# Kernel optimization log

Hardware: AMD Instinct MI355X
Metric: run time of the kernel (lower is better)

The kernel has to match this reference:

```python
import jax, jax.numpy as jnp
import numpy as np

TOK_DIM = 512
POS_DIM = 512
N_HEADS = 16
HEAD_DIM = 64
D_MODEL = 1024
INNER = N_HEADS * HEAD_DIM
B, T = 4, 2048


def setup_inputs() -> dict:
    key = jax.random.key(0)
    ks = jax.random.split(key, 5)
    s = 0.02
    return {
        "x": jax.random.normal(ks[0], (B, T, TOK_DIM + POS_DIM), dtype=jnp.float32),
        "Wq": jax.random.normal(ks[1], (POS_DIM, INNER), dtype=jnp.float32) * s,
        "Wk": jax.random.normal(ks[2], (POS_DIM, INNER), dtype=jnp.float32) * s,
        "Wv": jax.random.normal(ks[3], (TOK_DIM, INNER), dtype=jnp.float32) * s,
        "Wo": jax.random.normal(ks[4], (INNER, D_MODEL), dtype=jnp.float32) * s,
    }


def reference(x, Wq, Wk, Wv, Wo):
    b, t, _ = x.shape
    x_tok = x[:, :, :TOK_DIM]
    x_pos = x[:, :, TOK_DIM:]
    # project and split heads: [B, H, T, Dh]
    q = (x_pos @ Wq).reshape(b, t, N_HEADS, HEAD_DIM).transpose(0, 2, 1, 3)
    k = (x_pos @ Wk).reshape(b, t, N_HEADS, HEAD_DIM).transpose(0, 2, 1, 3)
    v = (x_tok @ Wv).reshape(b, t, N_HEADS, HEAD_DIM).transpose(0, 2, 1, 3)
    att = jnp.einsum("bhqd,bhkd->bhqk", q, k) / jnp.sqrt(jnp.float32(HEAD_DIM))
    causal = jnp.tril(jnp.ones((t, t), dtype=bool))
    att = jnp.where(causal, att, -jnp.inf)
    att = jax.nn.softmax(att, axis=-1)
    out = jnp.einsum("bhqk,bhkd->bhqd", att, v)
    out = out.transpose(0, 2, 1, 3).reshape(b, t, INNER)
    return out @ Wo
```

## Files before the change

### kernel.cpp

```cpp
#include <hip/hip_runtime.h>
#include <stdint.h>


typedef unsigned short u16;
typedef __bf16 bf16;
typedef bf16 bf16x8 __attribute__((ext_vector_type(8)));
typedef u16 u16x8 __attribute__((ext_vector_type(8)));
typedef u16 u16x4 __attribute__((ext_vector_type(4)));
typedef float f32x4 __attribute__((ext_vector_type(4)));
typedef uint32_t u32x4 __attribute__((ext_vector_type(4)));

__device__ __forceinline__ u16 cvt_bf16(float f) {
  uint32_t u = __builtin_bit_cast(uint32_t, f);
  u += 0x7FFFu + ((u >> 16) & 1u);
  return (u16)(u >> 16);
}

__device__ __forceinline__ f32x4 mfma_bf(bf16x8 a, bf16x8 b, f32x4 c) {
  return __builtin_amdgcn_mfma_f32_16x16x32_bf16(a, b, c, 0, 0, 0);
}

typedef __attribute__((address_space(1))) const uint32_t g_u32;
typedef __attribute__((address_space(3))) uint32_t l_u32;
__device__ __forceinline__ void gload16(const u16* g, u16* l) {
  __builtin_amdgcn_global_load_lds((g_u32*)g, (l_u32*)l, 16, 0, 0);
}

__global__ __launch_bounds__(256) void prep(
    const float* __restrict__ x, const float* __restrict__ Wq,
    const float* __restrict__ Wk, const float* __restrict__ Wv,
    const float* __restrict__ Wo, u16* __restrict__ xtok,
    u16* __restrict__ xpos, u16* __restrict__ Wt, u16* __restrict__ WoT) {
  const int gid = blockIdx.x;
  const int tid = threadIdx.x;
  if (gid < 1024) {
    const int z = gid >> 8;
    const float* src = (z == 0) ? Wq : (z == 1) ? Wk : (z == 2) ? Wv : Wo;
    const int K = (z == 3) ? 1024 : 512;
    u16* dst = (z == 3) ? WoT : (Wt + (size_t)z * 1024 * 512);
    const int k0 = ((gid >> 4) & 15) * 64, n0 = (gid & 15) * 64;
    if (k0 >= K) return;
    __shared__ u16 T[64][68];
    const int r = tid >> 4, c = (tid & 15) * 4;
#pragma unroll
    for (int i = 0; i < 4; i++) {
      float4 v = *(const float4*)(src + (size_t)(k0 + r + i * 16) * 1024 + n0 + c);
      u16x4 b = {cvt_bf16(v.x), cvt_bf16(v.y), cvt_bf16(v.z), cvt_bf16(v.w)};
      *(u16x4*)&T[r + i * 16][c] = b;
    }
    __syncthreads();
#pragma unroll
    for (int i = 0; i < 4; i++) {
      int n = r + i * 16;
      u16x4 v;
#pragma unroll
      for (int j = 0; j < 4; j++) v[j] = T[c + j][n];
      *(u16x4*)(dst + (size_t)(n0 + n) * K + k0 + c) = v;
    }
  } else {
    int idx = (gid - 1024) * 256 + tid;
    int row = idx >> 8;
    int c4 = (idx & 255) * 4;
    float4 v = *(const float4*)(x + (size_t)row * 1024 + c4);
    u16x4 b = {cvt_bf16(v.x), cvt_bf16(v.y), cvt_bf16(v.z), cvt_bf16(v.w)};
    u16* dst = (c4 < 512) ? (xtok + (size_t)row * 512 + c4)
                          : (xpos + (size_t)row * 512 + c4 - 512);
    *(u16x4*)dst = b;
  }
}


#define MM1(M_, N_, J_) { f32x4 c_ = acc[M_][N_];                            \
  c_ = mfma_bf(af[J_][0], bf[N_][0], c_);                                    \
  c_ = mfma_bf(af[J_][1], bf[N_][1], c_);                                    \
  acc[M_][N_] = c_; }

#define XMM(NB) MM1(0,(NB)+0,0) MM1(0,(NB)+1,0) MM1(1,(NB)+0,1)              \
                MM1(1,(NB)+1,1) MM1(2,(NB)+0,2) MM1(2,(NB)+1,2)              \
                MM1(3,(NB)+0,3) MM1(3,(NB)+1,3)

#define XLDA(P) { const u16* bp_ = rA + (P)*8192;                            \
  af[0][0] = *(const bf16x8*)(bp_ + 0*1024 + colx0);                         \
  af[0][1] = *(const bf16x8*)(bp_ + 0*1024 + colx1);                         \
  af[1][0] = *(const bf16x8*)(bp_ + 1*1024 + colx0);                         \
  af[1][1] = *(const bf16x8*)(bp_ + 1*1024 + colx1);                         \
  af[2][0] = *(const bf16x8*)(bp_ + 2*1024 + colx0);                         \
  af[2][1] = *(const bf16x8*)(bp_ + 2*1024 + colx1);                         \
  af[3][0] = *(const bf16x8*)(bp_ + 3*1024 + colx0);                         \
  af[3][1] = *(const bf16x8*)(bp_ + 3*1024 + colx1); }

#define XLDB(P, NB) { const u16* bp_ = rB + (P)*16384;                       \
  bf[(NB)+0][0] = *(const bf16x8*)(bp_ + ((NB)+0)*1024 + colx0);             \
  bf[(NB)+0][1] = *(const bf16x8*)(bp_ + ((NB)+0)*1024 + colx1);             \
  bf[(NB)+1][0] = *(const bf16x8*)(bp_ + ((NB)+1)*1024 + colx0);             \
  bf[(NB)+1][1] = *(const bf16x8*)(bp_ + ((NB)+1)*1024 + colx1); }

#define XSTA(P, KT) { const u16* s_ = gA + (KT)*64;                          \
  u16* d_ = lA + (P)*8192;                                                   \
  gload16(s_, d_); gload16(s_ + (size_t)64*Kd, d_ + 4096); }

#define XSTB0(P, KT) { const u16* s_ = gB + (KT)*64;                         \
  u16* d_ = lB + (P)*16384;                                                  \
  gload16(s_, d_); gload16(s_ + (size_t)64*Kd, d_ + 4096); }

#define XSTB1(P, KT) { const u16* s_ = gB + (size_t)128*Kd + (KT)*64;        \
  u16* d_ = lB + (P)*16384 + 8192;                                           \
  gload16(s_, d_); gload16(s_ + (size_t)64*Kd, d_ + 4096); }

#define PH_MID  asm volatile("" ::: "memory"); __builtin_amdgcn_s_barrier(); \
  asm volatile("s_waitcnt lgkmcnt(0)" ::: "memory");                         \
  __builtin_amdgcn_s_setprio(1);

#define PH_END_VM6  __builtin_amdgcn_s_setprio(0);                           \
  asm volatile("s_waitcnt vmcnt(6)" ::: "memory");                           \
  asm volatile("" ::: "memory"); __builtin_amdgcn_s_barrier();

template <int Kd>
__device__ __forceinline__ void gemm128_core(
    const u16* __restrict__ Aptr, const u16* __restrict__ Bptr,
    int m0, int n0, u16* smem, f32x4 (&acc)[4][4]) {
  constexpr int NKT = Kd / 64;
  const int tid = threadIdx.x;
  const int lane = tid & 63;
  const int mrow = lane & 15, quad = lane >> 4;
  const int w = tid >> 6, wm2 = w >> 2, wn4 = w & 3;

  u16* As = smem;
  u16* Bs = smem + 24576;

  const int lrs = tid >> 3, sp8 = tid & 7;
  const int slog = sp8 ^ (lrs & 7);
  const u16* gA = Aptr + (size_t)(m0 + lrs) * Kd + slog * 8;
  const u16* gB = Bptr + (size_t)(n0 + lrs) * Kd + slog * 8;
  u16* lA = As + tid * 8;
  u16* lB = Bs + tid * 8;

  const int colx0 = (quad * 8) ^ ((mrow & 7) * 8);
  const int colx1 = (32 + quad * 8) ^ ((mrow & 7) * 8);
  const u16* rA = As + (wm2 * 64 + mrow) * 64;
  const u16* rB = Bs + (wn4 >> 1) * 8192 + ((wn4 & 1) * 64 + mrow) * 64;

  bf16x8 af[4][2], bf[4][2];

  XSTA(0, 0) XSTB0(0, 0) XSTB1(0, 0)
  XSTA(1, 1) XSTB0(1, 1) XSTB1(1, 1)
  asm volatile("s_waitcnt vmcnt(6)" ::: "memory");
  asm volatile("" ::: "memory");
  __builtin_amdgcn_s_barrier();

  int p = 0, ps = 2;
  for (int t = 0; t < NKT; ++t) {
    const int kt = (t + 2 < NKT) ? t + 2 : NKT - 1;
    XLDA(p) XLDB(p, 0) XLDB(p, 2)
    XSTA(ps, kt) XSTB0(ps, kt) XSTB1(ps, kt)
    PH_MID
    XMM(0) XMM(2)
    PH_END_VM6
    p = (p == 2) ? 0 : p + 1;
    ps = (ps == 2) ? 0 : ps + 1;
  }
  asm volatile("s_waitcnt vmcnt(0)" ::: "memory");
  __builtin_amdgcn_s_barrier();
}

__device__ __forceinline__ void xcd_remap(int& bx, int& by) {
  int flat = blockIdx.x + 4 * blockIdx.y;
  int wg = (flat & 7) * 32 + (flat >> 3);
  bx = wg & 3;
  by = wg >> 2;
}

__global__ __launch_bounds__(512, 1) void gemm_qkv128(
    const u16* __restrict__ xtok, const u16* __restrict__ xpos,
    const u16* __restrict__ Wt, u16* __restrict__ qkv,
    u16* __restrict__ vperm) {
  const int z = blockIdx.z;
  const u16* A = (z == 2) ? xtok : xpos;
  const u16* Bt = Wt + (size_t)z * 1024 * 512;
  u16* outp = qkv + (size_t)z * (64u * 2048u * 64u);
  const float osc = (z == 0) ? 0.18033688011112042f : 1.0f;
  int bx, by;
  xcd_remap(bx, by);
  const int m0 = by * 128, n0 = bx * 256;

  __shared__ __align__(16) u16 smem[73728];
  f32x4 acc[4][4];
#pragma unroll
  for (int i = 0; i < 4; i++)
#pragma unroll
    for (int j = 0; j < 4; j++) acc[i][j] = (f32x4){0.f, 0.f, 0.f, 0.f};

  gemm128_core<512>(A, Bt, m0, n0, smem, acc);

  const int tid = threadIdx.x;
  const int lane = tid & 63;
  const int mrow = lane & 15, quad = lane >> 4;
  const int w = tid >> 6, wm2 = w >> 2, wn4 = w & 3;

  if (z != 2) {
#pragma unroll
    for (int mi = 0; mi < 4; mi++)
#pragma unroll
      for (int ni = 0; ni < 4; ni++)
#pragma unroll
        for (int r = 0; r < 4; r++) {
          int m = m0 + wm2 * 64 + mi * 16 + quad * 4 + r;
          int n = n0 + wn4 * 64 + ni * 16 + mrow;
          int bb = m >> 11, t = m & 2047;
          int h = n >> 6, d = n & 63;
          outp[(((size_t)(bb * 16 + h)) * 2048 + t) * 64 + d] =
              cvt_bf16(acc[mi][ni][r] * osc);
        }
  } else {
#pragma unroll
    for (int mi = 0; mi < 4; mi++)
#pragma unroll
      for (int ni = 0; ni < 4; ni++)
#pragma unroll
        for (int r = 0; r < 4; r++) {
          int m = m0 + wm2 * 64 + mi * 16 + quad * 4 + r;
          int n = n0 + wn4 * 64 + ni * 16 + mrow;
          int bb = m >> 11, t = m & 2047;
          int h = n >> 6, d = n & 63;
          int k6 = t & 63;
          int pos = (k6 & 32) + ((k6 >> 4) & 1) * 4 + ((k6 >> 2) & 3) * 8 +
                    (k6 & 3);
          vperm[(((size_t)(bb * 16 + h)) * 64 + d) * 2048 + (t & ~63) + pos] =
              cvt_bf16(acc[mi][ni][r]);
        }
  }
}

__global__ __launch_bounds__(512, 1) void gemm_out128(
    const u16* __restrict__ Am, const u16* __restrict__ WoT,
    float* __restrict__ out) {
  int bx, by;
  xcd_remap(bx, by);
  const int m0 = by * 128, n0 = bx * 256;

  __shared__ __align__(16) u16 smem[73728];
  f32x4 acc[4][4];
#pragma unroll
  for (int i = 0; i < 4; i++)
#pragma unroll
    for (int j = 0; j < 4; j++) acc[i][j] = (f32x4){0.f, 0.f, 0.f, 0.f};

  gemm128_core<1024>(Am, WoT, m0, n0, smem, acc);

  const int tid = threadIdx.x;
  const int lane = tid & 63;
  const int mrow = lane & 15, quad = lane >> 4;
  const int w = tid >> 6, wm2 = w >> 2, wn4 = w & 3;

#pragma unroll
  for (int mi = 0; mi < 4; mi++)
#pragma unroll
    for (int ni = 0; ni < 4; ni++)
#pragma unroll
      for (int r = 0; r < 4; r++) {
        int m = m0 + wm2 * 64 + mi * 16 + quad * 4 + r;
        int n = n0 + wn4 * 64 + ni * 16 + mrow;
        out[(size_t)m * 1024 + n] = acc[mi][ni][r];
      }
}

__global__ __launch_bounds__(256, 3) void attn(
    const u16* __restrict__ qkv, const u16* __restrict__ vperm,
    u16* __restrict__ aout) {
  const int bh = blockIdx.x;
  const int qt = 15 - blockIdx.y;
  const int bb = bh >> 4, h = bh & 15;
  const u16* Qp = qkv + (size_t)bh * (2048 * 64);
  const u16* Kp = qkv + (size_t)(64 + bh) * (2048 * 64);
  const u16* Vp = vperm + (size_t)bh * (64 * 2048);

  __shared__ __align__(16) u16 smem[2][4][64 * 32];

  const int tid = threadIdx.x;
  const int lane = tid & 63;
  const int w = tid >> 6;
  const int mrow = lane & 15;
  const int quad = lane >> 4;
  const int srow = w * 16 + (lane >> 2);
  const int sc = (lane & 3) * 8;
  const int soff = srow * 32 + sc;

  const u16x8 onesu = {0x3F80, 0x3F80, 0x3F80, 0x3F80,
                       0x3F80, 0x3F80, 0x3F80, 0x3F80};
  const bf16x8 ones = __builtin_bit_cast(bf16x8, onesu);

  const u16* kgb = Kp + (size_t)srow * 64 + sc;
  const u16* vgb = Vp + (size_t)srow * 2048 + sc;

  const int q0 = qt * 128;
  const int nk = 2 * qt + 2;
  const int qw = q0 + w * 32;

  const u16* qbase = Qp + (size_t)(qw + mrow) * 64 + quad * 8;
  const bf16x8 qf00 = *(const bf16x8*)qbase;
  const bf16x8 qf01 = *(const bf16x8*)(qbase + 32);
  const bf16x8 qf10 = *(const bf16x8*)(qbase + 16 * 64);
  const bf16x8 qf11 = *(const bf16x8*)(qbase + 16 * 64 + 32);

  f32x4 o[2][4], ol[2];
#pragma unroll
  for (int g = 0; g < 2; ++g) {
#pragma unroll
    for (int dt = 0; dt < 4; ++dt) o[g][dt] = (f32x4){0.f, 0.f, 0.f, 0.f};
    ol[g] = (f32x4){0.f, 0.f, 0.f, 0.f};
  }

  u16x8 ka0 = *(const u16x8*)kgb;
  u16x8 ka1 = *(const u16x8*)(kgb + 32);
  u16x8 va0 = *(const u16x8*)vgb;
  u16x8 va1 = *(const u16x8*)(vgb + 32);

  for (int it = 0; it < nk; ++it) {
    u16* buf = &smem[it & 1][0][0];
    *(u16x8*)(buf + 0 * 2048 + soff) = ka0;
    *(u16x8*)(buf + 1 * 2048 + soff) = ka1;
    *(u16x8*)(buf + 2 * 2048 + soff) = va0;
    *(u16x8*)(buf + 3 * 2048 + soff) = va1;

    if (it + 1 < nk) {
      const int kn = (it + 1) * 64;
      ka0 = *(const u16x8*)(kgb + (size_t)kn * 64);
      ka1 = *(const u16x8*)(kgb + (size_t)kn * 64 + 32);
      va0 = *(const u16x8*)(vgb + kn);
      va1 = *(const u16x8*)(vgb + kn + 32);
    }

    __syncthreads();

    const int k0 = it * 64;
    if (k0 > qw + 31) continue;

    f32x4 s[2][4];
#pragma unroll
    for (int nt = 0; nt < 4; ++nt) {
      bf16x8 kf0 = *(const bf16x8*)(buf + 0 * 2048 + (nt * 16 + mrow) * 32 + quad * 8);
      bf16x8 kf1 = *(const bf16x8*)(buf + 1 * 2048 + (nt * 16 + mrow) * 32 + quad * 8);
      f32x4 z0 = (f32x4){0.f, 0.f, 0.f, 0.f};
      z0 = mfma_bf(kf0, qf00, z0);
      s[0][nt] = mfma_bf(kf1, qf01, z0);
      f32x4 z1 = (f32x4){0.f, 0.f, 0.f, 0.f};
      z1 = mfma_bf(kf0, qf10, z1);
      s[1][nt] = mfma_bf(kf1, qf11, z1);
    }

    if (k0 + 63 > qw) {
#pragma unroll
      for (int g = 0; g < 2; ++g)
#pragma unroll
        for (int nt = 0; nt < 4; ++nt)
#pragma unroll
          for (int r = 0; r < 4; ++r)
            if (k0 + nt * 16 + quad * 4 + r > qw + g * 16 + mrow)
              s[g][nt][r] = -1e30f;
    }
#pragma unroll
    for (int g = 0; g < 2; ++g)
#pragma unroll
      for (int nt = 0; nt < 4; ++nt)
#pragma unroll
        for (int r = 0; r < 4; ++r)
          s[g][nt][r] = __builtin_amdgcn_exp2f(s[g][nt][r]);

    bf16x8 pf[2][2];
#pragma unroll
    for (int g = 0; g < 2; ++g) {
      pf[g][0] = (bf16x8){(bf16)s[g][0][0], (bf16)s[g][0][1],
                          (bf16)s[g][0][2], (bf16)s[g][0][3],
                          (bf16)s[g][1][0], (bf16)s[g][1][1],
                          (bf16)s[g][1][2], (bf16)s[g][1][3]};
      pf[g][1] = (bf16x8){(bf16)s[g][2][0], (bf16)s[g][2][1],
                          (bf16)s[g][2][2], (bf16)s[g][2][3],
                          (bf16)s[g][3][0], (bf16)s[g][3][1],
                          (bf16)s[g][3][2], (bf16)s[g][3][3]};
      ol[g] = mfma_bf(ones, pf[g][0], ol[g]);
      ol[g] = mfma_bf(ones, pf[g][1], ol[g]);
    }

#pragma unroll
    for (int dt = 0; dt < 4; ++dt) {
      bf16x8 vf0 = *(const bf16x8*)(buf + 2 * 2048 + (dt * 16 + mrow) * 32 + quad * 8);
      bf16x8 vf1 = *(const bf16x8*)(buf + 3 * 2048 + (dt * 16 + mrow) * 32 + quad * 8);
      o[0][dt] = mfma_bf(vf0, pf[0][0], o[0][dt]);
      o[0][dt] = mfma_bf(vf1, pf[0][1], o[0][dt]);
      o[1][dt] = mfma_bf(vf0, pf[1][0], o[1][dt]);
      o[1][dt] = mfma_bf(vf1, pf[1][1], o[1][dt]);
    }
  }

  __syncthreads();
  u16* Osh = &smem[0][0][0];

#pragma unroll
  for (int g = 0; g < 2; ++g) {
    const float inv = 1.f / ol[g][0];
#pragma unroll
    for (int dt = 0; dt < 4; ++dt)
#pragma unroll
      for (int r = 0; r < 4; ++r)
        Osh[(w * 32 + g * 16 + mrow) * 72 + dt * 16 + quad * 4 + r] =
            cvt_bf16(o[g][dt][r] * inv);
  }
#pragma unroll
  for (int p = 0; p < 4; ++p) {
    int ql = (lane >> 3) + 8 * p;
    int ch = lane & 7;
    u16x8 v = *(const u16x8*)&Osh[(w * 32 + ql) * 72 + ch * 8];
    int t = q0 + w * 32 + ql;
    *(u16x8*)(aout + ((size_t)(bb * 2048 + t)) * 1024 + h * 64 + ch * 8) = v;
  }
}

extern "C" void kernel_launch(void* const* d_in, const int* in_sizes, int n_in,
                              void* d_out, int out_size, void* d_ws, size_t ws_size,
                              hipStream_t stream) {
  const float* x  = (const float*)d_in[0];
  const float* Wq = (const float*)d_in[1];
  const float* Wk = (const float*)d_in[2];
  const float* Wv = (const float*)d_in[3];
  const float* Wo = (const float*)d_in[4];

  u16* qkv   = (u16*)d_ws;
  u16* vperm = qkv + (size_t)3 * 64 * 2048 * 64;
  u16* aout  = vperm + (size_t)64 * 64 * 2048;
  u16* xtok  = aout + (size_t)8192 * 1024;
  u16* xpos  = xtok + (size_t)8192 * 512;
  u16* Wt    = xpos + (size_t)8192 * 512;
  u16* WoT   = Wt + (size_t)3 * 1024 * 512;
  float* out = (float*)d_out;

  prep<<<dim3(1024 + 8192), dim3(256), 0, stream>>>(x, Wq, Wk, Wv, Wo, xtok,
                                                    xpos, Wt, WoT);
  gemm_qkv128<<<dim3(4, 64, 3), dim3(512), 0, stream>>>(xtok, xpos, Wt, qkv, vperm);
  attn<<<dim3(64, 16), dim3(256), 0, stream>>>(qkv, vperm, aout);
  gemm_out128<<<dim3(4, 64), dim3(512), 0, stream>>>(aout, WoT, out);
}
```

Measured before the change: 188.7 us.

## Shrink GEMM tiles to 128x128 with K=32 steps and higher occupancy

Reworks the shared GEMM core from 512-thread 128x256 tiles with 64-wide K steps to 256-thread 128x128 tiles with 32-wide K steps. The LDS swizzle, loads, MFMA schedule and XCD remap are changed to match, and launch bounds now allow three blocks per CU. The aim is more concurrent blocks to hide latency, using far less LDS per block. The cost is lower data reuse per tile and twice as many K iterations, each with its own barrier.

```diff
diff --git a/kernel.cpp b/kernel.cpp
--- a/kernel.cpp
+++ b/kernel.cpp
@@ -70,92 +70,89 @@
 }
 
 
-#define MM1(M_, N_, J_) { f32x4 c_ = acc[M_][N_];                            \
-  c_ = mfma_bf(af[J_][0], bf[N_][0], c_);                                    \
-  c_ = mfma_bf(af[J_][1], bf[N_][1], c_);                                    \
-  acc[M_][N_] = c_; }
-
-#define XMM(NB) MM1(0,(NB)+0,0) MM1(0,(NB)+1,0) MM1(1,(NB)+0,1)              \
-                MM1(1,(NB)+1,1) MM1(2,(NB)+0,2) MM1(2,(NB)+1,2)              \
-                MM1(3,(NB)+0,3) MM1(3,(NB)+1,3)
-
-#define XLDA(P) { const u16* bp_ = rA + (P)*8192;                            \
-  af[0][0] = *(const bf16x8*)(bp_ + 0*1024 + colx0);                         \
-  af[0][1] = *(const bf16x8*)(bp_ + 0*1024 + colx1);                         \
-  af[1][0] = *(const bf16x8*)(bp_ + 1*1024 + colx0);                         \
-  af[1][1] = *(const bf16x8*)(bp_ + 1*1024 + colx1);                         \
-  af[2][0] = *(const bf16x8*)(bp_ + 2*1024 + colx0);                         \
-  af[2][1] = *(const bf16x8*)(bp_ + 2*1024 + colx1);                         \
-  af[3][0] = *(const bf16x8*)(bp_ + 3*1024 + colx0);                         \
-  af[3][1] = *(const bf16x8*)(bp_ + 3*1024 + colx1); }
-
-#define XLDB(P, NB) { const u16* bp_ = rB + (P)*16384;                       \
-  bf[(NB)+0][0] = *(const bf16x8*)(bp_ + ((NB)+0)*1024 + colx0);             \
-  bf[(NB)+0][1] = *(const bf16x8*)(bp_ + ((NB)+0)*1024 + colx1);             \
-  bf[(NB)+1][0] = *(const bf16x8*)(bp_ + ((NB)+1)*1024 + colx0);             \
-  bf[(NB)+1][1] = *(const bf16x8*)(bp_ + ((NB)+1)*1024 + colx1); }
-
-#define XSTA(P, KT) { const u16* s_ = gA + (KT)*64;                          \
-  u16* d_ = lA + (P)*8192;                                                   \
-  gload16(s_, d_); gload16(s_ + (size_t)64*Kd, d_ + 4096); }
-
-#define XSTB0(P, KT) { const u16* s_ = gB + (KT)*64;                         \
-  u16* d_ = lB + (P)*16384;                                                  \
-  gload16(s_, d_); gload16(s_ + (size_t)64*Kd, d_ + 4096); }
-
-#define XSTB1(P, KT) { const u16* s_ = gB + (size_t)128*Kd + (KT)*64;        \
-  u16* d_ = lB + (P)*16384 + 8192;                                           \
-  gload16(s_, d_); gload16(s_ + (size_t)64*Kd, d_ + 4096); }
-
-#define PH_MID  asm volatile("" ::: "memory"); __builtin_amdgcn_s_barrier(); \
+#define YLD(P) {                                                             \
+  const u16* pa_ = rA + (P)*4096;                                            \
+  af[0] = *(const bf16x8*)(pa_ + 0*512 + colx);                              \
+  af[1] = *(const bf16x8*)(pa_ + 1*512 + colx);                              \
+  af[2] = *(const bf16x8*)(pa_ + 2*512 + colx);                              \
+  af[3] = *(const bf16x8*)(pa_ + 3*512 + colx);                              \
+  const u16* pb_ = rB + (P)*4096;                                            \
+  bf[0] = *(const bf16x8*)(pb_ + 0*512 + colx);                              \
+  bf[1] = *(const bf16x8*)(pb_ + 1*512 + colx);                              \
+  bf[2] = *(const bf16x8*)(pb_ + 2*512 + colx);                              \
+  bf[3] = *(const bf16x8*)(pb_ + 3*512 + colx); }
+
+#define YMM {                                                                \
+  acc[0][0] = mfma_bf(af[0], bf[0], acc[0][0]);                              \
+  acc[0][1] = mfma_bf(af[0], bf[1], acc[0][1]);                              \
+  acc[0][2] = mfma_bf(af[0], bf[2], acc[0][2]);                              \
+  acc[0][3] = mfma_bf(af[0], bf[3], acc[0][3]);                              \
+  acc[1][0] = mfma_bf(af[1], bf[0], acc[1][0]);                              \
+  acc[1][1] = mfma_bf(af[1], bf[1], acc[1][1]);                              \
+  acc[1][2] = mfma_bf(af[1], bf[2], acc[1][2]);                              \
+  acc[1][3] = mfma_bf(af[1], bf[3], acc[1][3]);                              \
+  acc[2][0] = mfma_bf(af[2], bf[0], acc[2][0]);                              \
+  acc[2][1] = mfma_bf(af[2], bf[1], acc[2][1]);                              \
+  acc[2][2] = mfma_bf(af[2], bf[2], acc[2][2]);                              \
+  acc[2][3] = mfma_bf(af[2], bf[3], acc[2][3]);                              \
+  acc[3][0] = mfma_bf(af[3], bf[0], acc[3][0]);                              \
+  acc[3][1] = mfma_bf(af[3], bf[1], acc[3][1]);                              \
+  acc[3][2] = mfma_bf(af[3], bf[2], acc[3][2]);                              \
+  acc[3][3] = mfma_bf(af[3], bf[3], acc[3][3]); }
+
+#define YST(P, KT) {                                                         \
+  gload16(gA + (KT)*32, lA + (P)*4096);                                      \
+  gload16(gA + (size_t)64*Kd + (KT)*32, lA + (P)*4096 + 2048);               \
+  gload16(gB + (KT)*32, lB + (P)*4096);                                      \
+  gload16(gB + (size_t)64*Kd + (KT)*32, lB + (P)*4096 + 2048); }
+
+#define YPH_MID  asm volatile("" ::: "memory"); __builtin_amdgcn_s_barrier();\
   asm volatile("s_waitcnt lgkmcnt(0)" ::: "memory");                         \
   __builtin_amdgcn_s_setprio(1);
 
-#define PH_END_VM6  __builtin_amdgcn_s_setprio(0);                           \
-  asm volatile("s_waitcnt vmcnt(6)" ::: "memory");                           \
+#define YPH_END  __builtin_amdgcn_s_setprio(0);                              \
+  asm volatile("s_waitcnt vmcnt(4)" ::: "memory");                           \
   asm volatile("" ::: "memory"); __builtin_amdgcn_s_barrier();
 
 template <int Kd>
 __device__ __forceinline__ void gemm128_core(
     const u16* __restrict__ Aptr, const u16* __restrict__ Bptr,
     int m0, int n0, u16* smem, f32x4 (&acc)[4][4]) {
-  constexpr int NKT = Kd / 64;
+  constexpr int NKT = Kd / 32;
   const int tid = threadIdx.x;
   const int lane = tid & 63;
   const int mrow = lane & 15, quad = lane >> 4;
-  const int w = tid >> 6, wm2 = w >> 2, wn4 = w & 3;
+  const int w = tid >> 6, wm = w >> 1, wn = w & 1;
 
   u16* As = smem;
-  u16* Bs = smem + 24576;
-
-  const int lrs = tid >> 3, sp8 = tid & 7;
-  const int slog = sp8 ^ (lrs & 7);
+  u16* Bs = smem + 12288;
+
+  const int lrs = tid >> 2, sp4 = tid & 3;
+  const int slog = sp4 ^ (lrs & 3);
   const u16* gA = Aptr + (size_t)(m0 + lrs) * Kd + slog * 8;
   const u16* gB = Bptr + (size_t)(n0 + lrs) * Kd + slog * 8;
   u16* lA = As + tid * 8;
   u16* lB = Bs + tid * 8;
 
-  const int colx0 = (quad * 8) ^ ((mrow & 7) * 8);
-  const int colx1 = (32 + quad * 8) ^ ((mrow & 7) * 8);
-  const u16* rA = As + (wm2 * 64 + mrow) * 64;
-  const u16* rB = Bs + (wn4 >> 1) * 8192 + ((wn4 & 1) * 64 + mrow) * 64;
-
-  bf16x8 af[4][2], bf[4][2];
-
-  XSTA(0, 0) XSTB0(0, 0) XSTB1(0, 0)
-  XSTA(1, 1) XSTB0(1, 1) XSTB1(1, 1)
-  asm volatile("s_waitcnt vmcnt(6)" ::: "memory");
+  const int colx = ((quad ^ (mrow & 3)) * 8);
+  const u16* rA = As + (wm * 64 + mrow) * 32;
+  const u16* rB = Bs + (wn * 64 + mrow) * 32;
+
+  bf16x8 af[4], bf[4];
+
+  YST(0, 0) YST(1, 1)
+  asm volatile("s_waitcnt vmcnt(4)" ::: "memory");
   asm volatile("" ::: "memory");
   __builtin_amdgcn_s_barrier();
 
   int p = 0, ps = 2;
   for (int t = 0; t < NKT; ++t) {
     const int kt = (t + 2 < NKT) ? t + 2 : NKT - 1;
-    XLDA(p) XLDB(p, 0) XLDB(p, 2)
-    XSTA(ps, kt) XSTB0(ps, kt) XSTB1(ps, kt)
-    PH_MID
-    XMM(0) XMM(2)
-    PH_END_VM6
+    YLD(p)
+    YST(ps, kt)
+    YPH_MID
+    YMM
+    YPH_END
     p = (p == 2) ? 0 : p + 1;
     ps = (ps == 2) ? 0 : ps + 1;
   }
@@ -164,13 +161,13 @@
 }
 
 __device__ __forceinline__ void xcd_remap(int& bx, int& by) {
-  int flat = blockIdx.x + 4 * blockIdx.y;
-  int wg = (flat & 7) * 32 + (flat >> 3);
-  bx = wg & 3;
-  by = wg >> 2;
-}
-
-__global__ __launch_bounds__(512, 1) void gemm_qkv128(
+  int flat = blockIdx.x + 8 * blockIdx.y;
+  int wg = (flat & 7) * 64 + (flat >> 3);
+  bx = wg & 7;
+  by = wg >> 3;
+}
+
+__global__ __launch_bounds__(256, 3) void gemm_qkv128(
     const u16* __restrict__ xtok, const u16* __restrict__ xpos,
     const u16* __restrict__ Wt, u16* __restrict__ qkv,
     u16* __restrict__ vperm) {
@@ -181,9 +178,9 @@
   const float osc = (z == 0) ? 0.18033688011112042f : 1.0f;
   int bx, by;
   xcd_remap(bx, by);
-  const int m0 = by * 128, n0 = bx * 256;
-
-  __shared__ __align__(16) u16 smem[73728];
+  const int m0 = by * 128, n0 = bx * 128;
+
+  __shared__ __align__(16) u16 smem[24576];
   f32x4 acc[4][4];
 #pragma unroll
   for (int i = 0; i < 4; i++)
@@ -195,7 +192,7 @@
   const int tid = threadIdx.x;
   const int lane = tid & 63;
   const int mrow = lane & 15, quad = lane >> 4;
-  const int w = tid >> 6, wm2 = w >> 2, wn4 = w & 3;
+  const int w = tid >> 6, wm = w >> 1, wn = w & 1;
 
   if (z != 2) {
 #pragma unroll
@@ -204,8 +201,8 @@
       for (int ni = 0; ni < 4; ni++)
 #pragma unroll
         for (int r = 0; r < 4; r++) {
-          int m = m0 + wm2 * 64 + mi * 16 + quad * 4 + r;
-          int n = n0 + wn4 * 64 + ni * 16 + mrow;
+          int m = m0 + wm * 64 + mi * 16 + quad * 4 + r;
+          int n = n0 + wn * 64 + ni * 16 + mrow;
           int bb = m >> 11, t = m & 2047;
           int h = n >> 6, d = n & 63;
           outp[(((size_t)(bb * 16 + h)) * 2048 + t) * 64 + d] =
@@ -218,8 +215,8 @@
       for (int ni = 0; ni < 4; ni++)
 #pragma unroll
         for (int r = 0; r < 4; r++) {
-          int m = m0 + wm2 * 64 + mi * 16 + quad * 4 + r;
-          int n = n0 + wn4 * 64 + ni * 16 + mrow;
+          int m = m0 + wm * 64 + mi * 16 + quad * 4 + r;
+          int n = n0 + wn * 64 + ni * 16 + mrow;
           int bb = m >> 11, t = m & 2047;
           int h = n >> 6, d = n & 63;
           int k6 = t & 63;
@@ -231,14 +228,14 @@
   }
 }
 
-__global__ __launch_bounds__(512, 1) void gemm_out128(
+__global__ __launch_bounds__(256, 3) void gemm_out128(
     const u16* __restrict__ Am, const u16* __restrict__ WoT,
     float* __restrict__ out) {
   int bx, by;
   xcd_remap(bx, by);
-  const int m0 = by * 128, n0 = bx * 256;
-
-  __shared__ __align__(16) u16 smem[73728];
+  const int m0 = by * 128, n0 = bx * 128;
+
+  __shared__ __align__(16) u16 smem[24576];
   f32x4 acc[4][4];
 #pragma unroll
   for (int i = 0; i < 4; i++)
@@ -250,7 +247,7 @@
   const int tid = threadIdx.x;
   const int lane = tid & 63;
   const int mrow = lane & 15, quad = lane >> 4;
-  const int w = tid >> 6, wm2 = w >> 2, wn4 = w & 3;
+  const int w = tid >> 6, wm = w >> 1, wn = w & 1;
 
 #pragma unroll
   for (int mi = 0; mi < 4; mi++)
@@ -258,8 +255,8 @@
     for (int ni = 0; ni < 4; ni++)
 #pragma unroll
       for (int r = 0; r < 4; r++) {
-        int m = m0 + wm2 * 64 + mi * 16 + quad * 4 + r;
-        int n = n0 + wn4 * 64 + ni * 16 + mrow;
+        int m = m0 + wm * 64 + mi * 16 + quad * 4 + r;
+        int n = n0 + wn * 64 + ni * 16 + mrow;
         out[(size_t)m * 1024 + n] = acc[mi][ni][r];
       }
 }
@@ -435,7 +432,7 @@
 
   prep<<<dim3(1024 + 8192), dim3(256), 0, stream>>>(x, Wq, Wk, Wv, Wo, xtok,
                                                     xpos, Wt, WoT);
-  gemm_qkv128<<<dim3(4, 64, 3), dim3(512), 0, stream>>>(xtok, xpos, Wt, qkv, vperm);
+  gemm_qkv128<<<dim3(8, 64, 3), dim3(256), 0, stream>>>(xtok, xpos, Wt, qkv, vperm);
   attn<<<dim3(64, 16), dim3(256), 0, stream>>>(qkv, vperm, aout);
-  gemm_out128<<<dim3(4, 64), dim3(512), 0, stream>>>(aout, WoT, out);
-}
+  gemm_out128<<<dim3(8, 64), dim3(256), 0, stream>>>(aout, WoT, out);
+}
```

Result: no change. 189.1 us (median of 2 runs) (+0.2%).
